# Kernel tuning notes

Hardware: AMD Instinct MI355X
Metric: run time of the kernel (lower is better)

## Reference

```python
import jax, jax.numpy as jnp
import numpy as np

B, L1, L2 = 16, 32, 128
DEC = 512       # decoder_size
MEM = 512       # memory_bank_size
TOP = 50        # topic_num


def setup_inputs() -> dict:
    key = jax.random.key(0)
    ks = jax.random.split(key, 16)
    s = lambda fan_in: 1.0 / np.sqrt(fan_in)
    inp = {
        "decoder_state": jax.random.normal(ks[0], (B, DEC), jnp.float32),
        "doc_memory": jax.random.normal(ks[1], (B, L1, MEM), jnp.float32),
        "word_memory": jax.random.normal(ks[2], (B, L1, L2, MEM), jnp.float32),
        "topic_dist": jax.random.uniform(ks[3], (B, TOP), jnp.float32),
        "doc_mask": jnp.ones((B, L1), jnp.int32),
        "word_mask": jnp.ones((B, L1, L2), jnp.int32),
        # HierAttention params (PyTorch Linear weight layout: [out, in])
        "Wv": jax.random.uniform(ks[4], (1, DEC), jnp.float32, -s(DEC), s(DEC)),
        "Wd": jax.random.uniform(ks[5], (DEC, DEC), jnp.float32, -s(DEC), s(DEC)),
        "Wt": jax.random.uniform(ks[6], (DEC, TOP), jnp.float32, -s(TOP), s(TOP)),
        "Wm": jax.random.uniform(ks[7], (DEC, MEM), jnp.float32, -s(MEM), s(MEM)),
        # doc_attention (inner Attention) params
        "Wv2": jax.random.uniform(ks[8], (1, DEC), jnp.float32, -s(DEC), s(DEC)),
        "Wd2": jax.random.uniform(ks[9], (DEC, DEC), jnp.float32, -s(DEC), s(DEC)),
        "Wt2": jax.random.uniform(ks[10], (DEC, TOP), jnp.float32, -s(TOP), s(TOP)),
        "Wm2": jax.random.uniform(ks[11], (DEC, MEM), jnp.float32, -s(MEM), s(MEM)),
    }
    return inp


def reference(decoder_state, doc_memory, word_memory, topic_dist,
              doc_mask, word_mask,
              Wv, Wd, Wt, Wm, Wv2, Wd2, Wt2, Wm2):
    neg_inf = jnp.float32(-jnp.inf)

    # ---- word-level (HierAttention.score) ----
    enc_feat = jnp.einsum('bqwm,dm->bqwd', word_memory, Wm)      # [B,L1,L2,DEC]
    dec_feat = decoder_state @ Wd.T                              # [B,DEC]
    top_feat = topic_dist @ Wt.T                                 # [B,DEC]
    e = jnp.tanh(enc_feat + (dec_feat + top_feat)[:, None, None, :])
    word_scores = jnp.einsum('bqwd,od->bqw', e, Wv)[..., 0] if Wv.shape[0] != 1 else jnp.einsum('bqwd,d->bqw', e, Wv[0])
    word_scores = jnp.where(word_mask == 0, neg_inf, word_scores)
    word_attn = jax.nn.softmax(word_scores, axis=-1)             # [B,L1,L2]

    # ---- doc-level (Attention.score) ----
    enc_feat_d = jnp.einsum('bqm,dm->bqd', doc_memory, Wm2)      # [B,L1,DEC]
    dec_feat_d = decoder_state @ Wd2.T                           # [B,DEC]
    top_feat_d = topic_dist @ Wt2.T                              # [B,DEC]
    e_d = jnp.tanh(enc_feat_d + (dec_feat_d + top_feat_d)[:, None, :])
    doc_scores = jnp.einsum('bqd,d->bq', e_d, Wv2[0])            # [B,L1]
    doc_scores = jnp.where(doc_mask == 0, neg_inf, doc_scores)
    doc_attn = jax.nn.softmax(doc_scores, axis=-1)               # [B,L1]

    # ---- combine ----
    rescaled = doc_attn[..., None] * word_attn                   # [B,L1,L2]
    context = jnp.einsum('bqw,bqwm->bm', rescaled, word_memory)  # [B,MEM]
    return context, rescaled
```

## Files before the change

### kernel.cpp

```cpp
#include <hip/hip_runtime.h>
#include <hip/hip_bf16.h>
#include <math.h>

#define BATCH 16
#define L1 32
#define L2 128
#define DEC 512
#define MEM 512
#define TOPN 50
#define NROWS (BATCH * L1 * L2)
#define NBQ (BATCH * L1)

typedef short short8 __attribute__((ext_vector_type(8)));
typedef float f32x16 __attribute__((ext_vector_type(16)));

#define WS_WP     0
#define WS_WP2    131072
#define WS_BIAS1  262144
#define WS_BIAS2  270336
#define WS_DOCSC  278528
#define WS_DOCAT  279040
#define WS_CTXP   279552

__device__ __forceinline__ unsigned int pkbf(float a, float b) {
    __hip_bfloat162 h = __float22bfloat162_rn(float2{a, b});
    union { __hip_bfloat162 h; unsigned int u; } c{h};
    return c.u;
}

__device__ __forceinline__ float fast_tanh(float x) {
    return 1.f - 2.f / (__expf(2.f * x) + 1.f);
}

__global__ __launch_bounds__(256) void setup_kernel(
    const float* __restrict__ Wm, const float* __restrict__ Wm2,
    unsigned short* __restrict__ Wp, unsigned short* __restrict__ Wp2,
    const float* __restrict__ dec, const float* __restrict__ topic,
    const float* __restrict__ Wd, const float* __restrict__ Wt,
    const float* __restrict__ Wd2, const float* __restrict__ Wt2,
    float* __restrict__ bias1, float* __restrict__ bias2)
{
    if (blockIdx.x < 128) {
        int s = blockIdx.x * 256 + threadIdx.x;
        int C = s >> 10;
        int u = s & 1023;
        int nt = u >> 6, k8 = (u >> 5) & 1, n_in = u & 31;
        int d = nt * 32 + n_in;
        int k = C * 16 + k8 * 8;

        const float* src = Wm + (size_t)d * DEC + k;
        uint4 v;
        v.x = pkbf(src[0], src[1]); v.y = pkbf(src[2], src[3]);
        v.z = pkbf(src[4], src[5]); v.w = pkbf(src[6], src[7]);
        ((uint4*)Wp)[s] = v;

        const float* src2 = Wm2 + (size_t)d * DEC + k;
        uint4 w;
        w.x = pkbf(src2[0], src2[1]); w.y = pkbf(src2[2], src2[3]);
        w.z = pkbf(src2[4], src2[5]); w.w = pkbf(src2[6], src2[7]);
        ((uint4*)Wp2)[s] = w;
    } else {
        int idx = (blockIdx.x - 128) * 256 + threadIdx.x;
        int b = idx >> 9, d = idx & 511;
        float a1 = 0.f, a2 = 0.f;
        const float* db = dec + b * DEC;
        const float* w1 = Wd + (size_t)d * DEC;
        const float* w2 = Wd2 + (size_t)d * DEC;
#pragma unroll 4
        for (int k = 0; k < DEC; ++k) {
            float x = db[k];
            a1 = fmaf(x, w1[k], a1);
            a2 = fmaf(x, w2[k], a2);
        }
        const float* tb = topic + b * TOPN;
        const float* t1 = Wt + (size_t)d * TOPN;
        const float* t2 = Wt2 + (size_t)d * TOPN;
#pragma unroll 2
        for (int t = 0; t < TOPN; ++t) {
            float x = tb[t];
            a1 = fmaf(x, t1[t], a1);
            a2 = fmaf(x, t2[t], a2);
        }
        bias1[idx] = a1;
        bias2[idx] = a2;
    }
}

__global__ __launch_bounds__(256) void score_mfma_kernel(
    const float* __restrict__ X,
    const unsigned short* __restrict__ Wp,
    const float* __restrict__ Wv,
    const float* __restrict__ bias,
    float* __restrict__ scores,
    int bshift)
{
    __shared__ __align__(16) short lsA[256 * 8];
    __shared__ __align__(16) short lsB[2048 * 8];
    __shared__ float red[4][64];

    const int tid = threadIdx.x;
    const int lane = tid & 63;
    const int wid = tid >> 6;
    const int row0 = blockIdx.x * 64;

    const int srow = tid >> 2;
    const int kslot = tid & 3;
    const int sA = ((kslot >> 1) * 2 + (srow >> 5)) * 64 + (kslot & 1) * 32 + (srow & 31);
    const float4* xs4 = (const float4*)(X + (size_t)(row0 + srow) * DEC) + kslot * 2;

    const uint4* bsrc = (const uint4*)Wp + (size_t)wid * 512 + lane;

    f32x16 acc[8];
#pragma unroll
    for (int t = 0; t < 8; ++t)
        acc[t] = (f32x16){0.f,0.f,0.f,0.f, 0.f,0.f,0.f,0.f, 0.f,0.f,0.f,0.f, 0.f,0.f,0.f,0.f};

    const short8* lA = (const short8*)lsA;
    const short8* lB = (const short8*)lsB;

    for (int it = 0; it < 16; ++it) {
        uint4 bv[8];
#pragma unroll
        for (int i = 0; i < 8; ++i) bv[i] = bsrc[i * 64];
        bsrc += 2048;
#pragma unroll
        for (int i = 0; i < 8; ++i)
            *((uint4*)&lsB[((size_t)wid * 512 + i * 64 + lane) * 8]) = bv[i];

        float4 xv0 = xs4[0];
        float4 xv1 = xs4[1];
        xs4 += 8;
        union { unsigned int u[4]; short8 s; } xb;
        xb.u[0] = pkbf(xv0.x, xv0.y); xb.u[1] = pkbf(xv0.z, xv0.w);
        xb.u[2] = pkbf(xv1.x, xv1.y); xb.u[3] = pkbf(xv1.z, xv1.w);
        *((short8*)&lsA[sA * 8]) = xb.s;

        __syncthreads();

#pragma unroll
        for (int c = 0; c < 2; ++c) {
            short8 a0 = lA[(c * 2 + 0) * 64 + lane];
            short8 a1 = lA[(c * 2 + 1) * 64 + lane];
            short8 b0 = lB[c * 1024 + (wid * 4 + 0) * 64 + lane];
            short8 b1 = lB[c * 1024 + (wid * 4 + 1) * 64 + lane];
            short8 b2 = lB[c * 1024 + (wid * 4 + 2) * 64 + lane];
            short8 b3 = lB[c * 1024 + (wid * 4 + 3) * 64 + lane];
            acc[0] = __builtin_amdgcn_mfma_f32_32x32x16_bf16(a0, b0, acc[0], 0, 0, 0);
            acc[1] = __builtin_amdgcn_mfma_f32_32x32x16_bf16(a0, b1, acc[1], 0, 0, 0);
            acc[2] = __builtin_amdgcn_mfma_f32_32x32x16_bf16(a0, b2, acc[2], 0, 0, 0);
            acc[3] = __builtin_amdgcn_mfma_f32_32x32x16_bf16(a0, b3, acc[3], 0, 0, 0);
            acc[4] = __builtin_amdgcn_mfma_f32_32x32x16_bf16(a1, b0, acc[4], 0, 0, 0);
            acc[5] = __builtin_amdgcn_mfma_f32_32x32x16_bf16(a1, b1, acc[5], 0, 0, 0);
            acc[6] = __builtin_amdgcn_mfma_f32_32x32x16_bf16(a1, b2, acc[6], 0, 0, 0);
            acc[7] = __builtin_amdgcn_mfma_f32_32x32x16_bf16(a1, b3, acc[7], 0, 0, 0);
        }
        __syncthreads();
    }

    const int col = lane & 31;
    const int h = lane >> 5;
    float wv[4], bs[2][4];
    const int b0i = (row0) >> bshift;
    const int b1i = (row0 + 32) >> bshift;
#pragma unroll
    for (int nt = 0; nt < 4; ++nt) {
        int d = wid * 128 + nt * 32 + col;
        wv[nt] = Wv[d];
        bs[0][nt] = bias[b0i * DEC + d];
        bs[1][nt] = bias[b1i * DEC + d];
    }

#pragma unroll
    for (int mt = 0; mt < 2; ++mt) {
#pragma unroll
        for (int r = 0; r < 16; ++r) {
            float p = 0.f;
#pragma unroll
            for (int nt = 0; nt < 4; ++nt) {
                float x = acc[mt * 4 + nt][r] + bs[mt][nt];
                p = fmaf(wv[nt], fast_tanh(x), p);
            }
            p += __shfl_xor(p, 16);
            p += __shfl_xor(p, 8);
            p += __shfl_xor(p, 4);
            p += __shfl_xor(p, 2);
            p += __shfl_xor(p, 1);
            if (col == mt * 16 + r) {
                int row_in = (r & 3) + 8 * (r >> 2) + 4 * h;
                red[wid][mt * 32 + row_in] = p;
            }
        }
    }
    __syncthreads();
    if (tid < 64)
        scores[row0 + tid] = red[0][tid] + red[1][tid] + red[2][tid] + red[3][tid];
}

__global__ __launch_bounds__(512) void doc_softmax_kernel(
    const float* __restrict__ doc_scores, const int* __restrict__ doc_mask,
    float* __restrict__ doc_attn)
{
    int tid = threadIdx.x;
    float s = doc_scores[tid];
    if (doc_mask[tid] == 0) s = -INFINITY;
    float mx = s;
#pragma unroll
    for (int o = 1; o <= 16; o <<= 1) mx = fmaxf(mx, __shfl_xor(mx, o));
    float e = __expf(s - mx);
    float sum = e;
#pragma unroll
    for (int o = 1; o <= 16; o <<= 1) sum += __shfl_xor(sum, o);
    doc_attn[tid] = e / sum;
}

__global__ __launch_bounds__(512) void fused_word_kernel(
    const float* __restrict__ X,
    const unsigned short* __restrict__ Wp,
    const float* __restrict__ Wv,
    const float* __restrict__ bias1,
    const float* __restrict__ doc_attn,
    const int* __restrict__ word_mask,
    float* __restrict__ rescaled_out,
    float* __restrict__ ctx_part)
{
    __shared__ __align__(16) short lsA[2 * 2048];
    __shared__ float red[8][128];
    __shared__ float sS[128];
    __shared__ float rmax2[2], rsum2[2];
    __shared__ __align__(16) float4 part[3 * 128];

    const int tid = threadIdx.x;
    const int lane = tid & 63;
    const int wid = tid >> 6;
    const int bq = blockIdx.x;
    const int r0 = bq * L2;
    const int b = bq >> 5;

    const int row = tid >> 2;
    const int kq = tid & 3;
    const int mt_s = row >> 5;
    const int rl_s = row & 31;
    const int k8_s = kq >> 1;
    const int q4 = (kq & 1) * 4;
    const int slot_s = mt_s * 64 + k8_s * 32 + rl_s;
    const float4* xs = (const float4*)(X + (size_t)(r0 + row) * DEC) + kq;

    const uint4* Bp = (const uint4*)Wp;
    const int boff = wid * 128 + lane;

    f32x16 acc[8];
#pragma unroll
    for (int t = 0; t < 8; ++t)
        acc[t] = (f32x16){0.f,0.f,0.f,0.f, 0.f,0.f,0.f,0.f, 0.f,0.f,0.f,0.f, 0.f,0.f,0.f,0.f};

    const short8* lA = (const short8*)lsA;

    float4 va = xs[0];
    uint4 ub0 = Bp[boff];
    uint4 ub1 = Bp[boff + 64];

    for (int c = 0; c < 32; ++c) {
        const int p = c & 1;
        uint2 wv2;
        wv2.x = pkbf(va.x, va.y);
        wv2.y = pkbf(va.z, va.w);
        *(uint2*)&lsA[(p * 256 + slot_s) * 8 + q4] = wv2;
        __syncthreads();

        const int c2 = (c + 1) & 31;
        float4 vnext = xs[c2 * 4];
        uint4 nb0 = Bp[c2 * 1024 + boff];
        uint4 nb1 = Bp[c2 * 1024 + boff + 64];

        short8 a0 = lA[p * 256 + 0 * 64 + lane];
        short8 a1 = lA[p * 256 + 1 * 64 + lane];
        short8 a2 = lA[p * 256 + 2 * 64 + lane];
        short8 a3 = lA[p * 256 + 3 * 64 + lane];
        union { uint4 u; short8 s; } cb0{ub0}, cb1{ub1};
        acc[0] = __builtin_amdgcn_mfma_f32_32x32x16_bf16(a0, cb0.s, acc[0], 0, 0, 0);
        acc[1] = __builtin_amdgcn_mfma_f32_32x32x16_bf16(a0, cb1.s, acc[1], 0, 0, 0);
        acc[2] = __builtin_amdgcn_mfma_f32_32x32x16_bf16(a1, cb0.s, acc[2], 0, 0, 0);
        acc[3] = __builtin_amdgcn_mfma_f32_32x32x16_bf16(a1, cb1.s, acc[3], 0, 0, 0);
        acc[4] = __builtin_amdgcn_mfma_f32_32x32x16_bf16(a2, cb0.s, acc[4], 0, 0, 0);
        acc[5] = __builtin_amdgcn_mfma_f32_32x32x16_bf16(a2, cb1.s, acc[5], 0, 0, 0);
        acc[6] = __builtin_amdgcn_mfma_f32_32x32x16_bf16(a3, cb0.s, acc[6], 0, 0, 0);
        acc[7] = __builtin_amdgcn_mfma_f32_32x32x16_bf16(a3, cb1.s, acc[7], 0, 0, 0);

        va = vnext; ub0 = nb0; ub1 = nb1;
    }

    const int col = lane & 31;
    const int h = lane >> 5;
    float wv0, wv1, bs0, bs1;
    {
        int d0 = wid * 64 + col;
        int d1 = wid * 64 + 32 + col;
        wv0 = Wv[d0]; wv1 = Wv[d1];
        bs0 = bias1[b * DEC + d0]; bs1 = bias1[b * DEC + d1];
    }
#pragma unroll
    for (int mt = 0; mt < 4; ++mt) {
#pragma unroll
        for (int r = 0; r < 16; ++r) {
            float p = fmaf(wv0, fast_tanh(acc[mt * 2 + 0][r] + bs0),
                           wv1 * fast_tanh(acc[mt * 2 + 1][r] + bs1));
            p += __shfl_xor(p, 16);
            p += __shfl_xor(p, 8);
            p += __shfl_xor(p, 4);
            p += __shfl_xor(p, 2);
            p += __shfl_xor(p, 1);
            if (col == r) {
                int row_in = (r & 3) + 8 * (r >> 2) + 4 * h;
                red[wid][mt * 32 + row_in] = p;
            }
        }
    }
    __syncthreads();

    float e = 0.f, sv = 0.f;
    if (tid < 128) {
        sv = red[0][tid] + red[1][tid] + red[2][tid] + red[3][tid]
           + red[4][tid] + red[5][tid] + red[6][tid] + red[7][tid];
        if (word_mask[r0 + tid] == 0) sv = -INFINITY;
        float mx = sv;
#pragma unroll
        for (int o = 1; o <= 32; o <<= 1) mx = fmaxf(mx, __shfl_xor(mx, o));
        if (lane == 0) rmax2[wid] = mx;
    }
    __syncthreads();
    if (tid < 128) {
        float mx = fmaxf(rmax2[0], rmax2[1]);
        e = __expf(sv - mx);
        float sum = e;
#pragma unroll
        for (int o = 1; o <= 32; o <<= 1) sum += __shfl_xor(sum, o);
        if (lane == 0) rsum2[wid] = sum;
    }
    __syncthreads();
    if (tid < 128) {
        float sum = rsum2[0] + rsum2[1];
        float resc = doc_attn[bq] * (e / sum);
        sS[tid] = resc;
        rescaled_out[r0 + tid] = resc;
    }
    __syncthreads();

    const int hh = tid >> 7;
    const int m4 = tid & 127;
    const float4* Xr = (const float4*)X + (size_t)r0 * 128 + (size_t)hh * 32 * 128 + m4;
    float4 a = {0.f, 0.f, 0.f, 0.f};
#pragma unroll 8
    for (int i = 0; i < 32; ++i) {
        float rr = sS[hh * 32 + i];
        float4 v = Xr[(size_t)i * 128];
        a.x = fmaf(rr, v.x, a.x);
        a.y = fmaf(rr, v.y, a.y);
        a.z = fmaf(rr, v.z, a.z);
        a.w = fmaf(rr, v.w, a.w);
    }
    if (hh) part[(hh - 1) * 128 + m4] = a;
    __syncthreads();
    if (hh == 0) {
        float4 p0 = part[m4], p1 = part[128 + m4], p2 = part[256 + m4];
        a.x += p0.x + p1.x + p2.x;
        a.y += p0.y + p1.y + p2.y;
        a.z += p0.z + p1.z + p2.z;
        a.w += p0.w + p1.w + p2.w;
        *(float4*)(ctx_part + (size_t)bq * MEM + m4 * 4) = a;
    }
}

__global__ __launch_bounds__(256) void ctx_reduce_kernel(
    const float* __restrict__ ctx_part,
    float* __restrict__ ctx_out)
{
    int idx = blockIdx.x * 256 + threadIdx.x;
    int b = idx >> 9, m = idx & 511;
    float s = 0.f;
#pragma unroll
    for (int q = 0; q < L1; ++q)
        s += ctx_part[(size_t)(b * L1 + q) * MEM + m];
    ctx_out[idx] = s;
}

extern "C" void kernel_launch(void* const* d_in, const int* in_sizes, int n_in,
                              void* d_out, int out_size, void* d_ws, size_t ws_size,
                              hipStream_t stream) {
    const float* decoder_state = (const float*)d_in[0];
    const float* doc_memory    = (const float*)d_in[1];
    const float* word_memory   = (const float*)d_in[2];
    const float* topic_dist    = (const float*)d_in[3];
    const int*   doc_mask      = (const int*)d_in[4];
    const int*   word_mask     = (const int*)d_in[5];
    const float* Wv  = (const float*)d_in[6];
    const float* Wd  = (const float*)d_in[7];
    const float* Wt  = (const float*)d_in[8];
    const float* Wm  = (const float*)d_in[9];
    const float* Wv2 = (const float*)d_in[10];
    const float* Wd2 = (const float*)d_in[11];
    const float* Wt2 = (const float*)d_in[12];
    const float* Wm2 = (const float*)d_in[13];

    float* ws = (float*)d_ws;
    unsigned short* Wp  = (unsigned short*)(ws + WS_WP);
    unsigned short* Wp2 = (unsigned short*)(ws + WS_WP2);
    float* bias1       = ws + WS_BIAS1;
    float* bias2       = ws + WS_BIAS2;
    float* doc_scores  = ws + WS_DOCSC;
    float* doc_attn    = ws + WS_DOCAT;
    float* ctx_part    = ws + WS_CTXP;

    float* ctx_out      = (float*)d_out;
    float* rescaled_out = (float*)d_out + BATCH * MEM;

    setup_kernel<<<160, 256, 0, stream>>>(Wm, Wm2, Wp, Wp2,
                                          decoder_state, topic_dist,
                                          Wd, Wt, Wd2, Wt2, bias1, bias2);
    score_mfma_kernel<<<NBQ / 64, 256, 0, stream>>>(doc_memory, Wp2, Wv2, bias2, doc_scores, 5);
    doc_softmax_kernel<<<1, 512, 0, stream>>>(doc_scores, doc_mask, doc_attn);
    fused_word_kernel<<<NBQ, 512, 0, stream>>>(word_memory, Wp, Wv, bias1,
                                               doc_attn, word_mask, rescaled_out, ctx_part);
    ctx_reduce_kernel<<<32, 256, 0, stream>>>(ctx_part, ctx_out);
}
```

Measured before the change: 368.3 us.

## Fuse doc softmax and context reduction into word kernel, deepen prefetch

Removes the separate doc-softmax and ctx-reduce kernels. Each word block now recomputes its batch's 32-way doc softmax locally and adds its partial context straight into the output with float atomics, after the setup kernel zeroes that output. The MFMA main loop is fully unrolled and prefetches X four chunks ahead and weights two chunks ahead instead of one. This saves two launches and a workspace round trip, at the cost of atomic contention, non-deterministic summation order, and more register pressure.

```diff
diff --git a/kernel.cpp b/kernel.cpp
--- a/kernel.cpp
+++ b/kernel.cpp
@@ -19,8 +19,6 @@
 #define WS_BIAS1  262144
 #define WS_BIAS2  270336
 #define WS_DOCSC  278528
-#define WS_DOCAT  279040
-#define WS_CTXP   279552
 
 __device__ __forceinline__ unsigned int pkbf(float a, float b) {
     __hip_bfloat162 h = __float22bfloat162_rn(float2{a, b});
@@ -38,7 +36,8 @@
     const float* __restrict__ dec, const float* __restrict__ topic,
     const float* __restrict__ Wd, const float* __restrict__ Wt,
     const float* __restrict__ Wd2, const float* __restrict__ Wt2,
-    float* __restrict__ bias1, float* __restrict__ bias2)
+    float* __restrict__ bias1, float* __restrict__ bias2,
+    float* __restrict__ ctx_out)
 {
     if (blockIdx.x < 128) {
         int s = blockIdx.x * 256 + threadIdx.x;
@@ -59,7 +58,7 @@
         w.x = pkbf(src2[0], src2[1]); w.y = pkbf(src2[2], src2[3]);
         w.z = pkbf(src2[4], src2[5]); w.w = pkbf(src2[6], src2[7]);
         ((uint4*)Wp2)[s] = w;
-    } else {
+    } else if (blockIdx.x < 160) {
         int idx = (blockIdx.x - 128) * 256 + threadIdx.x;
         int b = idx >> 9, d = idx & 511;
         float a1 = 0.f, a2 = 0.f;
@@ -83,6 +82,11 @@
         }
         bias1[idx] = a1;
         bias2[idx] = a2;
+    } else {
+        int i = (blockIdx.x - 160) * 256 + threadIdx.x;
+        float4 z = {0.f, 0.f, 0.f, 0.f};
+        ((float4*)ctx_out)[i * 2] = z;
+        ((float4*)ctx_out)[i * 2 + 1] = z;
     }
 }
 
@@ -196,37 +200,22 @@
         scores[row0 + tid] = red[0][tid] + red[1][tid] + red[2][tid] + red[3][tid];
 }
 
-__global__ __launch_bounds__(512) void doc_softmax_kernel(
-    const float* __restrict__ doc_scores, const int* __restrict__ doc_mask,
-    float* __restrict__ doc_attn)
-{
-    int tid = threadIdx.x;
-    float s = doc_scores[tid];
-    if (doc_mask[tid] == 0) s = -INFINITY;
-    float mx = s;
-#pragma unroll
-    for (int o = 1; o <= 16; o <<= 1) mx = fmaxf(mx, __shfl_xor(mx, o));
-    float e = __expf(s - mx);
-    float sum = e;
-#pragma unroll
-    for (int o = 1; o <= 16; o <<= 1) sum += __shfl_xor(sum, o);
-    doc_attn[tid] = e / sum;
-}
-
 __global__ __launch_bounds__(512) void fused_word_kernel(
     const float* __restrict__ X,
     const unsigned short* __restrict__ Wp,
     const float* __restrict__ Wv,
     const float* __restrict__ bias1,
-    const float* __restrict__ doc_attn,
+    const float* __restrict__ doc_scores,
+    const int* __restrict__ doc_mask,
     const int* __restrict__ word_mask,
     float* __restrict__ rescaled_out,
-    float* __restrict__ ctx_part)
+    float* __restrict__ ctx_out)
 {
     __shared__ __align__(16) short lsA[2 * 2048];
     __shared__ float red[8][128];
     __shared__ float sS[128];
     __shared__ float rmax2[2], rsum2[2];
+    __shared__ float s_dattn;
     __shared__ __align__(16) float4 part[3 * 128];
 
     const int tid = threadIdx.x;
@@ -235,6 +224,21 @@
     const int bq = blockIdx.x;
     const int r0 = bq * L2;
     const int b = bq >> 5;
+    const int q = bq & 31;
+
+    if (tid < 32) {
+        int di = b * 32 + tid;
+        float dsv = doc_scores[di];
+        if (doc_mask[di] == 0) dsv = -INFINITY;
+        float mx = dsv;
+#pragma unroll
+        for (int o = 1; o <= 16; o <<= 1) mx = fmaxf(mx, __shfl_xor(mx, o));
+        float e = __expf(dsv - mx);
+        float sum = e;
+#pragma unroll
+        for (int o = 1; o <= 16; o <<= 1) sum += __shfl_xor(sum, o);
+        if (tid == q) s_dattn = e / sum;
+    }
 
     const int row = tid >> 2;
     const int kq = tid & 3;
@@ -255,28 +259,35 @@
 
     const short8* lA = (const short8*)lsA;
 
-    float4 va = xs[0];
-    uint4 ub0 = Bp[boff];
-    uint4 ub1 = Bp[boff + 64];
-
+    float4 va[4];
+#pragma unroll
+    for (int i = 0; i < 4; ++i) va[i] = xs[i * 4];
+    uint4 ub0[2], ub1[2];
+#pragma unroll
+    for (int i = 0; i < 2; ++i) {
+        ub0[i] = Bp[i * 1024 + boff];
+        ub1[i] = Bp[i * 1024 + boff + 64];
+    }
+
+#pragma unroll
     for (int c = 0; c < 32; ++c) {
         const int p = c & 1;
-        uint2 wv2;
-        wv2.x = pkbf(va.x, va.y);
-        wv2.y = pkbf(va.z, va.w);
-        *(uint2*)&lsA[(p * 256 + slot_s) * 8 + q4] = wv2;
+        const int ia = c & 3;
+        uint2 w2;
+        w2.x = pkbf(va[ia].x, va[ia].y);
+        w2.y = pkbf(va[ia].z, va[ia].w);
+        *(uint2*)&lsA[(p * 256 + slot_s) * 8 + q4] = w2;
         __syncthreads();
 
-        const int c2 = (c + 1) & 31;
-        float4 vnext = xs[c2 * 4];
-        uint4 nb0 = Bp[c2 * 1024 + boff];
-        uint4 nb1 = Bp[c2 * 1024 + boff + 64];
+        va[ia] = xs[((c + 4) & 31) * 4];
+        uint4 nb0 = Bp[((c + 2) & 31) * 1024 + boff];
+        uint4 nb1 = Bp[((c + 2) & 31) * 1024 + boff + 64];
 
         short8 a0 = lA[p * 256 + 0 * 64 + lane];
         short8 a1 = lA[p * 256 + 1 * 64 + lane];
         short8 a2 = lA[p * 256 + 2 * 64 + lane];
         short8 a3 = lA[p * 256 + 3 * 64 + lane];
-        union { uint4 u; short8 s; } cb0{ub0}, cb1{ub1};
+        union { uint4 u; short8 s; } cb0{ub0[p]}, cb1{ub1[p]};
         acc[0] = __builtin_amdgcn_mfma_f32_32x32x16_bf16(a0, cb0.s, acc[0], 0, 0, 0);
         acc[1] = __builtin_amdgcn_mfma_f32_32x32x16_bf16(a0, cb1.s, acc[1], 0, 0, 0);
         acc[2] = __builtin_amdgcn_mfma_f32_32x32x16_bf16(a1, cb0.s, acc[2], 0, 0, 0);
@@ -286,7 +297,7 @@
         acc[6] = __builtin_amdgcn_mfma_f32_32x32x16_bf16(a3, cb0.s, acc[6], 0, 0, 0);
         acc[7] = __builtin_amdgcn_mfma_f32_32x32x16_bf16(a3, cb1.s, acc[7], 0, 0, 0);
 
-        va = vnext; ub0 = nb0; ub1 = nb1;
+        ub0[p] = nb0; ub1[p] = nb1;
     }
 
     const int col = lane & 31;
@@ -339,7 +350,7 @@
     __syncthreads();
     if (tid < 128) {
         float sum = rsum2[0] + rsum2[1];
-        float resc = doc_attn[bq] * (e / sum);
+        float resc = s_dattn * (e / sum);
         sS[tid] = resc;
         rescaled_out[r0 + tid] = resc;
     }
@@ -366,21 +377,12 @@
         a.y += p0.y + p1.y + p2.y;
         a.z += p0.z + p1.z + p2.z;
         a.w += p0.w + p1.w + p2.w;
-        *(float4*)(ctx_part + (size_t)bq * MEM + m4 * 4) = a;
-    }
-}
-
-__global__ __launch_bounds__(256) void ctx_reduce_kernel(
-    const float* __restrict__ ctx_part,
-    float* __restrict__ ctx_out)
-{
-    int idx = blockIdx.x * 256 + threadIdx.x;
-    int b = idx >> 9, m = idx & 511;
-    float s = 0.f;
-#pragma unroll
-    for (int q = 0; q < L1; ++q)
-        s += ctx_part[(size_t)(b * L1 + q) * MEM + m];
-    ctx_out[idx] = s;
+        float* dst = ctx_out + (size_t)b * MEM + m4 * 4;
+        atomicAdd(dst + 0, a.x);
+        atomicAdd(dst + 1, a.y);
+        atomicAdd(dst + 2, a.z);
+        atomicAdd(dst + 3, a.w);
+    }
 }
 
 extern "C" void kernel_launch(void* const* d_in, const int* in_sizes, int n_in,
@@ -407,18 +409,15 @@
     float* bias1       = ws + WS_BIAS1;
     float* bias2       = ws + WS_BIAS2;
     float* doc_scores  = ws + WS_DOCSC;
-    float* doc_attn    = ws + WS_DOCAT;
-    float* ctx_part    = ws + WS_CTXP;
 
     float* ctx_out      = (float*)d_out;
     float* rescaled_out = (float*)d_out + BATCH * MEM;
 
-    setup_kernel<<<160, 256, 0, stream>>>(Wm, Wm2, Wp, Wp2,
+    setup_kernel<<<164, 256, 0, stream>>>(Wm, Wm2, Wp, Wp2,
                                           decoder_state, topic_dist,
-                                          Wd, Wt, Wd2, Wt2, bias1, bias2);
+                                          Wd, Wt, Wd2, Wt2, bias1, bias2, ctx_out);
     score_mfma_kernel<<<NBQ / 64, 256, 0, stream>>>(doc_memory, Wp2, Wv2, bias2, doc_scores, 5);
-    doc_softmax_kernel<<<1, 512, 0, stream>>>(doc_scores, doc_mask, doc_attn);
     fused_word_kernel<<<NBQ, 512, 0, stream>>>(word_memory, Wp, Wv, bias1,
-                                               doc_attn, word_mask, rescaled_out, ctx_part);
-    ctx_reduce_kernel<<<32, 256, 0, stream>>>(ctx_part, ctx_out);
-}
+                                               doc_scores, doc_mask, word_mask,
+                                               rescaled_out, ctx_out);
+}
```

After: 351.7 us. 4.5% less time.
